# Optimization experiments

Measured on AMD Instinct MI355X. Metric: run time of the kernel, lower is better.

Reference implementation:

```python
import jax, jax.numpy as jnp
import numpy as np

N = 50000
E = 400000
F_IN = 128
HID = 64
HEADS = 4
OUT_HEADS = 4
N_CLS = 121
NEG_SLOPE = 0.2


def _gat_layer(x, src, dst, W, a_src, a_dst, b, heads, out_ch, concat):
    n = x.shape[0]
    xh = (x @ W).reshape(n, heads, out_ch)                      # [N,H,C]
    alpha_s = jnp.sum(xh * a_src, axis=-1)                      # [N,H]
    alpha_d = jnp.sum(xh * a_dst, axis=-1)                      # [N,H]
    logits = jax.nn.leaky_relu(alpha_s[src] + alpha_d[dst], NEG_SLOPE)  # [E,H]
    # numerically stable edge softmax per destination node
    m = jax.ops.segment_max(logits, dst, num_segments=n)        # [N,H]
    e = jnp.exp(logits - m[dst])                                # [E,H]
    denom = jax.ops.segment_sum(e, dst, num_segments=n)         # [N,H]
    alpha = e / (denom[dst] + 1e-16)                            # [E,H]
    msg = alpha[:, :, None] * xh[src]                           # [E,H,C]
    out = jax.ops.segment_sum(msg, dst, num_segments=n)         # [N,H,C]
    if concat:
        out = out.reshape(n, heads * out_ch)
    else:
        out = out.mean(axis=1)
    return out + b


def setup_inputs() -> dict:
    key = jax.random.key(0)
    ks = jax.random.split(key, 20)
    x = jax.random.normal(ks[0], (N, F_IN), dtype=jnp.float32)
    edge_index = jax.random.randint(ks[1], (2, E), 0, N, dtype=jnp.int32)
    s = lambda *sh: 1.0 / np.sqrt(sh[0])
    inp = {
        'x': x,
        'edge_index': edge_index,
        # conv1: F_IN -> HEADS*HID
        'W1': jax.random.normal(ks[2], (F_IN, HEADS * HID), jnp.float32) * s(F_IN),
        'a1_src': jax.random.normal(ks[3], (HEADS, HID), jnp.float32) * s(HID),
        'a1_dst': jax.random.normal(ks[4], (HEADS, HID), jnp.float32) * s(HID),
        'b1': jnp.zeros((HEADS * HID,), jnp.float32),
        'lin1_W': jax.random.normal(ks[5], (F_IN, HEADS * HID), jnp.float32) * s(F_IN),
        'lin1_b': jnp.zeros((HEADS * HID,), jnp.float32),
        # conv2: HEADS*HID -> HEADS*HID
        'W2': jax.random.normal(ks[6], (HEADS * HID, HEADS * HID), jnp.float32) * s(HEADS * HID),
        'a2_src': jax.random.normal(ks[7], (HEADS, HID), jnp.float32) * s(HID),
        'a2_dst': jax.random.normal(ks[8], (HEADS, HID), jnp.float32) * s(HID),
        'b2': jnp.zeros((HEADS * HID,), jnp.float32),
        # conv3: HEADS*HID -> N_CLS (mean over OUT_HEADS)
        'W3': jax.random.normal(ks[9], (HEADS * HID, OUT_HEADS * N_CLS), jnp.float32) * s(HEADS * HID),
        'a3_src': jax.random.normal(ks[10], (OUT_HEADS, N_CLS), jnp.float32) * s(N_CLS),
        'a3_dst': jax.random.normal(ks[11], (OUT_HEADS, N_CLS), jnp.float32) * s(N_CLS),
        'b3': jnp.zeros((N_CLS,), jnp.float32),
        'lin3_W': jax.random.normal(ks[12], (HEADS * HID, N_CLS), jnp.float32) * s(HEADS * HID),
        'lin3_b': jnp.zeros((N_CLS,), jnp.float32),
    }
    return inp


def reference(x, edge_index, W1, a1_src, a1_dst, b1, lin1_W, lin1_b,
              W2, a2_src, a2_dst, b2, W3, a3_src, a3_dst, b3, lin3_W, lin3_b):
    src, dst = edge_index[0], edge_index[1]
    h = _gat_layer(x, src, dst, W1, a1_src, a1_dst, b1, HEADS, HID, True) + (x @ lin1_W + lin1_b)
    h = jax.nn.elu(h)
    h = _gat_layer(h, src, dst, W2, a2_src, a2_dst, b2, HEADS, HID, True) + h  # residual skip (no lin2)
    h = jax.nn.elu(h)
    out = _gat_layer(h, src, dst, W3, a3_src, a3_dst, b3, OUT_HEADS, N_CLS, False) + (h @ lin3_W + lin3_b)
    return out
```

## Files before the change

kernel.cpp:

```cpp
#include <hip/hip_runtime.h>
#include <cstdint>
#include <cstddef>

#define F_IN 128
#define HC12 256
#define HC3 484
#define HC3P 488
#define NCLS 121

typedef unsigned short u16;
typedef unsigned int u32;
typedef __attribute__((ext_vector_type(8))) short short8;
typedef __attribute__((ext_vector_type(8))) __fp16 half8;
typedef __attribute__((ext_vector_type(4))) float float4v;

static __device__ __forceinline__ float lrelu(float x) { return x > 0.f ? x : 0.2f * x; }

static __device__ __forceinline__ u16 f2h(float f) {
    union { __fp16 h; u16 u; } v; v.h = (__fp16)f; return v.u;
}
static __device__ __forceinline__ float h2f(u16 u) {
    union { u16 u; __fp16 h; } v; v.u = u; return (float)v.h;
}

static __device__ __forceinline__ void gload16(const u16* g, u16* l) {
    __builtin_amdgcn_global_load_lds((const __attribute__((address_space(1))) void*)g,
                                     (__attribute__((address_space(3))) void*)l,
                                     16, 0, 0);
}

__global__ void hist_kernel(const int* __restrict__ dst, int* __restrict__ deg, int E) {
    int e = blockIdx.x * 256 + threadIdx.x;
    if (e < E) atomicAdd(&deg[dst[e]], 1);
}

__global__ __launch_bounds__(1024) void scan_kernel(const int* __restrict__ deg,
                                                    int* __restrict__ rowp, int N) {
    __shared__ int swave[16];
    __shared__ int s_carry;
    int tid = threadIdx.x;
    int w = tid >> 6, lane = tid & 63;
    if (tid == 0) { rowp[0] = 0; s_carry = 0; }
    __syncthreads();
    for (int base = 0; base < N; base += 4096) {
        int i0 = base + tid * 4;
        int v0 = (i0     < N) ? deg[i0]     : 0;
        int v1 = (i0 + 1 < N) ? deg[i0 + 1] : 0;
        int v2 = (i0 + 2 < N) ? deg[i0 + 2] : 0;
        int v3 = (i0 + 3 < N) ? deg[i0 + 3] : 0;
        int t = v0 + v1 + v2 + v3;
        int sc = t;
#pragma unroll
        for (int off = 1; off < 64; off <<= 1) {
            int u = __shfl_up(sc, off, 64);
            if (lane >= off) sc += u;
        }
        if (lane == 63) swave[w] = sc;
        __syncthreads();
        if (w == 0) {
            int ws = (lane < 16) ? swave[lane] : 0;
#pragma unroll
            for (int off = 1; off < 16; off <<= 1) {
                int u = __shfl_up(ws, off, 64);
                if (lane >= off) ws += u;
            }
            if (lane < 16) swave[lane] = ws;
        }
        __syncthreads();
        int carry = s_carry;
        int tb = carry + ((w > 0) ? swave[w - 1] : 0) + sc - t;
        if (i0     < N) rowp[i0 + 1] = tb + v0;
        if (i0 + 1 < N) rowp[i0 + 2] = tb + v0 + v1;
        if (i0 + 2 < N) rowp[i0 + 3] = tb + v0 + v1 + v2;
        if (i0 + 3 < N) rowp[i0 + 4] = tb + t;
        __syncthreads();
        if (tid == 1023) s_carry = carry + swave[15];
        __syncthreads();
    }
}

__global__ void scatter_kernel(const int* __restrict__ src, const int* __restrict__ dst,
                               const int* __restrict__ rowp, int* __restrict__ cur,
                               int* __restrict__ col, int E) {
    int e = blockIdx.x * 256 + threadIdx.x;
    if (e < E) {
        int d = dst[e];
        int pos = rowp[d] + atomicAdd(&cur[d], 1);
        col[pos] = src[e];
    }
}

__global__ void cvtT_all_kernel(const float* W1, const float* l1W, const float* W2,
                                const float* W3, const float* l3W,
                                u16* C1, u16* C2, u16* C3) {
    int i = blockIdx.x * 256 + threadIdx.x;
    const float* B; u16* o; int K, N;
    if (i < 32768)       { B = W1;  o = C1;             K = 128; N = 256; }
    else if (i < 65536)  { B = l1W; o = C1 + 256 * 128; K = 128; N = 256; i -= 32768; }
    else if (i < 131072) { B = W2;  o = C2;             K = 256; N = 256; i -= 65536; }
    else if (i < 254976) { B = W3;  o = C3;             K = 256; N = 484; i -= 131072; }
    else if (i < 285952) { B = l3W; o = C3 + 484 * 256; K = 256; N = 121; i -= 254976; }
    else return;
    int n = i % N, k = i / N;
    o[(size_t)n * K + k] = f2h(B[(size_t)k * N + n]);
}

__global__ __launch_bounds__(256) void xcvt_kernel(const float* __restrict__ x,
                                                   u16* __restrict__ o, int total8) {
    int i = blockIdx.x * 256 + threadIdx.x;
    if (i >= total8) return;
    const float4* p = (const float4*)(x + (size_t)i * 8);
    float4 a = p[0], b = p[1];
    union { u16 u[8]; short8 v; } r;
    r.u[0] = f2h(a.x); r.u[1] = f2h(a.y); r.u[2] = f2h(a.z); r.u[3] = f2h(a.w);
    r.u[4] = f2h(b.x); r.u[5] = f2h(b.y); r.u[6] = f2h(b.z); r.u[7] = f2h(b.w);
    *(short8*)(o + (size_t)i * 8) = r.v;
}

#define BM 128
#define BN 128
#define BK 32

__global__ __launch_bounds__(256, 3) void gemm_f16(const u16* __restrict__ A16,
                                                   const u16* __restrict__ BT,
                                                   int M, int K, int Ntot,
                                                   int nx, int ny,
                                                   int Nb, u16* __restrict__ Cb, int strideB,
                                                   int pad121,
                                                   float* __restrict__ Cf,
                                                   const float* __restrict__ biasf, int strideF) {
    __shared__ __align__(16) u16 sA[BM * BK];
    __shared__ __align__(16) u16 sB[BN * BK];
    int tid = threadIdx.x;
    int wave = tid >> 6, lane = tid & 63;
    int wr = wave >> 1, wc = wave & 1;

    int bid = blockIdx.x;
    int G = nx * 8;
    int g = bid / G;
    int rem = ny - g * 8;
    int rb, cb;
    if (rem >= 8) {
        int r = bid - g * G;
        rb = g * 8 + (r & 7);
        cb = r >> 3;
    } else {
        int t = bid - g * G;
        rb = g * 8 + t % rem;
        cb = t / rem;
    }
    int m0 = rb * BM, n0 = cb * BN;

    int fm = lane & 15;
    int q = lane >> 4;

    int srow = lane >> 2;
    int sch = (lane & 3) * 8;
    u16* lA0 = &sA[(wave * 32) * BK];
    u16* lA1 = &sA[(wave * 32 + 16) * BK];
    u16* lB0 = &sB[(wave * 32) * BK];
    u16* lB1 = &sB[(wave * 32 + 16) * BK];
    int ar0 = min(m0 + wave * 32 + srow, M - 1);
    int ar1 = min(m0 + wave * 32 + 16 + srow, M - 1);
    int br0 = min(n0 + wave * 32 + srow, Ntot - 1);
    int br1 = min(n0 + wave * 32 + 16 + srow, Ntot - 1);

    float4v acc[4][4];
#pragma unroll
    for (int i = 0; i < 4; i++)
#pragma unroll
        for (int j = 0; j < 4; j++) acc[i][j] = (float4v){0.f, 0.f, 0.f, 0.f};

    for (int kc = 0; kc < K; kc += BK) {
        gload16(&A16[(size_t)ar0 * K + kc + sch], lA0);
        gload16(&A16[(size_t)ar1 * K + kc + sch], lA1);
        gload16(&BT[(size_t)br0 * K + kc + sch], lB0);
        gload16(&BT[(size_t)br1 * K + kc + sch], lB1);
        __syncthreads();

        half8 ah[4];
#pragma unroll
        for (int mi = 0; mi < 4; mi++)
            ah[mi] = *(const half8*)&sA[(wr * 64 + mi * 16 + fm) * BK + q * 8];
#pragma unroll
        for (int ni = 0; ni < 4; ni++) {
            half8 bh = *(const half8*)&sB[(wc * 64 + ni * 16 + fm) * BK + q * 8];
#pragma unroll
            for (int mi = 0; mi < 4; mi++)
                acc[mi][ni] = __builtin_amdgcn_mfma_f32_16x16x32_f16(ah[mi], bh, acc[mi][ni], 0, 0, 0);
        }
        __syncthreads();
    }

#pragma unroll
    for (int mi = 0; mi < 4; mi++) {
#pragma unroll
        for (int ni = 0; ni < 4; ni++) {
            int colg = n0 + wc * 64 + ni * 16 + fm;
            if (colg >= Ntot) continue;
            int cg = colg;
            if (pad121 && colg < Nb) {
                int hh = (colg * 1084) >> 17;
                cg = colg + hh;
            }
#pragma unroll
            for (int r = 0; r < 4; r++) {
                int rowg = m0 + wr * 64 + mi * 16 + q * 4 + r;
                if (rowg >= M) continue;
                float v = acc[mi][ni][r];
                if (colg < Nb) {
                    Cb[(size_t)rowg * strideB + cg] = f2h(v);
                } else {
                    int cf = colg - Nb;
                    Cf[(size_t)rowg * strideF + cf] = v + biasf[cf];
                }
            }
        }
    }
}

__global__ __launch_bounds__(256) void alpha_wave_256(const u16* __restrict__ xh,
                                                      const float* __restrict__ a_s,
                                                      const float* __restrict__ a_d,
                                                      float* __restrict__ as_o,
                                                      float* __restrict__ ad_o, int N) {
    int lane = threadIdx.x & 63;
    int n = blockIdx.x * 4 + (threadIdx.x >> 6);
    if (n >= N) return;
    int c = lane * 4;
    uint2 v = *(const uint2*)&xh[(size_t)n * HC12 + c];
    float4 s4 = *(const float4*)&a_s[c];
    float4 d4 = *(const float4*)&a_d[c];
    float x0 = h2f((u16)(v.x & 0xffff)), x1 = h2f((u16)(v.x >> 16));
    float x2 = h2f((u16)(v.y & 0xffff)), x3 = h2f((u16)(v.y >> 16));
    float ss = x0 * s4.x + x1 * s4.y + x2 * s4.z + x3 * s4.w;
    float sd = x0 * d4.x + x1 * d4.y + x2 * d4.z + x3 * d4.w;
#pragma unroll
    for (int o = 1; o < 16; o <<= 1) {
        ss += __shfl_xor(ss, o, 64);
        sd += __shfl_xor(sd, o, 64);
    }
    if ((lane & 15) == 0) {
        as_o[n * 4 + (lane >> 4)] = ss;
        ad_o[n * 4 + (lane >> 4)] = sd;
    }
}

__global__ __launch_bounds__(256) void alpha3_wave(const u16* __restrict__ xh3,
                                                   const float* __restrict__ a_s,
                                                   const float* __restrict__ a_d,
                                                   float* __restrict__ as_o,
                                                   float* __restrict__ ad_o, int N) {
    int lane = threadIdx.x & 63;
    int n = blockIdx.x * 4 + (threadIdx.x >> 6);
    if (n >= N) return;
    int l = min(lane, 60);
    int c0 = 2 * l;
    float m0 = (lane < 61) ? 1.f : 0.f;
    float m1 = (lane < 61 && c0 + 1 < NCLS) ? 1.f : 0.f;
    int d1 = (c0 + 1 < NCLS) ? 1 : 0;
    const u16* row = xh3 + (size_t)n * HC3P;
    float ss[4], sd[4];
#pragma unroll
    for (int h = 0; h < 4; h++) {
        u32 v = *(const u32*)&row[h * 122 + c0];
        float x0 = h2f((u16)(v & 0xffff)) * m0;
        float x1 = h2f((u16)(v >> 16)) * m1;
        int i0 = h * NCLS + c0;
        ss[h] = x0 * a_s[i0] + x1 * a_s[i0 + d1];
        sd[h] = x0 * a_d[i0] + x1 * a_d[i0 + d1];
    }
#pragma unroll
    for (int o = 1; o < 64; o <<= 1) {
#pragma unroll
        for (int h = 0; h < 4; h++) {
            ss[h] += __shfl_xor(ss[h], o, 64);
            sd[h] += __shfl_xor(sd[h], o, 64);
        }
    }
    if (lane == 0) {
#pragma unroll
        for (int h = 0; h < 4; h++) {
            as_o[n * 4 + h] = ss[h];
            ad_o[n * 4 + h] = sd[h];
        }
    }
}

__global__ __launch_bounds__(256) void stats_alpha_kernel(const int* __restrict__ rowp,
                                                          const int* __restrict__ col,
                                                          const float* __restrict__ asrc,
                                                          const float* __restrict__ adst,
                                                          float* __restrict__ alphaE, int N) {
    int i = blockIdx.x * 256 + threadIdx.x;
    if (i >= N * 4) return;
    int n = i >> 2, h = i & 3;
    int r0 = rowp[n], r1 = rowp[n + 1];
    float ad = adst[i];
    float m = -3.4e38f, s = 0.f;
    for (int e = r0; e < r1; e++) {
        int sc = col[e];
        float l = lrelu(asrc[sc * 4 + h] + ad);
        float nm = fmaxf(m, l);
        s = s * __expf(m - nm) + __expf(l - nm);
        m = nm;
    }
    float rd = 1.f / (s + 1e-16f);
    for (int e = r0; e < r1; e++) {
        int sc = col[e];
        float l = lrelu(asrc[sc * 4 + h] + ad);
        alphaE[(size_t)e * 4 + h] = __expf(l - m) * rd;
    }
}

__global__ __launch_bounds__(256) void agg_wave_256(const u16* __restrict__ xh,
                                                    const int* __restrict__ rowp,
                                                    const int* __restrict__ col,
                                                    const float* __restrict__ alphaE,
                                                    const float* __restrict__ bias,
                                                    const float* __restrict__ res,
                                                    float* __restrict__ outf,
                                                    u16* __restrict__ out16, int N) {
    int lane = threadIdx.x & 63;
    int n = blockIdx.x * 4 + (threadIdx.x >> 6);
    if (n >= N) return;
    int r0 = rowp[n], r1 = rowp[n + 1];
    int c = lane * 4;
    int h = lane >> 4;
    float a0 = 0.f, a1 = 0.f, a2 = 0.f, a3 = 0.f;
    for (int kb = r0; kb < r1; kb += 16) {
        int cn = min(16, r1 - kb);
        int cidx = col[kb + (lane & 15)];
        float alv = alphaE[(size_t)kb * 4 + lane];
#pragma unroll 4
        for (int k = 0; k < cn; k++) {
            int src = __shfl(cidx, k, 64);
            float al = __shfl(alv, k * 4 + h, 64);
            uint2 v = *(const uint2*)&xh[(size_t)src * HC12 + c];
            a0 += al * h2f((u16)(v.x & 0xffff));
            a1 += al * h2f((u16)(v.x >> 16));
            a2 += al * h2f((u16)(v.y & 0xffff));
            a3 += al * h2f((u16)(v.y >> 16));
        }
    }
    float4 bv = *(const float4*)&bias[c];
    float4 rv = *(const float4*)&res[(size_t)n * HC12 + c];
    float v0 = a0 + bv.x + rv.x;
    float v1 = a1 + bv.y + rv.y;
    float v2 = a2 + bv.z + rv.z;
    float v3 = a3 + bv.w + rv.w;
    float e0 = v0 > 0.f ? v0 : expm1f(v0);
    float e1 = v1 > 0.f ? v1 : expm1f(v1);
    float e2 = v2 > 0.f ? v2 : expm1f(v2);
    float e3 = v3 > 0.f ? v3 : expm1f(v3);
    if (outf) {
        float4 o4; o4.x = e0; o4.y = e1; o4.z = e2; o4.w = e3;
        *(float4*)&outf[(size_t)n * HC12 + c] = o4;
    }
    union { u16 u[4]; uint2 v; } p;
    p.u[0] = f2h(e0); p.u[1] = f2h(e1); p.u[2] = f2h(e2); p.u[3] = f2h(e3);
    *(uint2*)&out16[(size_t)n * HC12 + c] = p.v;
}

__global__ __launch_bounds__(256) void agg_wave_out(const u16* __restrict__ xh3,
                                                    const int* __restrict__ rowp,
                                                    const int* __restrict__ col,
                                                    const float* __restrict__ alphaE,
                                                    const float* __restrict__ b3,
                                                    const float* __restrict__ lin3,
                                                    float* __restrict__ out, int N) {
    int lane = threadIdx.x & 63;
    int n = blockIdx.x * 4 + (threadIdx.x >> 6);
    if (n >= N) return;
    int r0 = rowp[n], r1 = rowp[n + 1];
    int l = min(lane, 60);
    int c0 = 2 * l;
    float acc[4][2];
#pragma unroll
    for (int h = 0; h < 4; h++) { acc[h][0] = 0.f; acc[h][1] = 0.f; }
    for (int kb = r0; kb < r1; kb += 16) {
        int cn = min(16, r1 - kb);
        int cidx = col[kb + (lane & 15)];
        float alv = alphaE[(size_t)kb * 4 + lane];
#pragma unroll 4
        for (int k = 0; k < cn; k++) {
            int src = __shfl(cidx, k, 64);
            float al0 = __shfl(alv, k * 4 + 0, 64);
            float al1 = __shfl(alv, k * 4 + 1, 64);
            float al2 = __shfl(alv, k * 4 + 2, 64);
            float al3 = __shfl(alv, k * 4 + 3, 64);
            const u16* row = xh3 + (size_t)src * HC3P + c0;
            u32 v0 = *(const u32*)&row[0];
            u32 v1 = *(const u32*)&row[122];
            u32 v2 = *(const u32*)&row[244];
            u32 v3 = *(const u32*)&row[366];
            acc[0][0] += al0 * h2f((u16)(v0 & 0xffff));
            acc[0][1] += al0 * h2f((u16)(v0 >> 16));
            acc[1][0] += al1 * h2f((u16)(v1 & 0xffff));
            acc[1][1] += al1 * h2f((u16)(v1 >> 16));
            acc[2][0] += al2 * h2f((u16)(v2 & 0xffff));
            acc[2][1] += al2 * h2f((u16)(v2 >> 16));
            acc[3][0] += al3 * h2f((u16)(v3 & 0xffff));
            acc[3][1] += al3 * h2f((u16)(v3 >> 16));
        }
    }
    if (lane < 61) {
        float o0 = 0.25f * (acc[0][0] + acc[1][0] + acc[2][0] + acc[3][0])
                   + b3[c0] + lin3[(size_t)n * NCLS + c0];
        out[(size_t)n * NCLS + c0] = o0;
        if (c0 + 1 < NCLS) {
            float o1 = 0.25f * (acc[0][1] + acc[1][1] + acc[2][1] + acc[3][1])
                       + b3[c0 + 1] + lin3[(size_t)n * NCLS + c0 + 1];
            out[(size_t)n * NCLS + c0 + 1] = o1;
        }
    }
}

extern "C" void kernel_launch(void* const* d_in, const int* in_sizes, int n_in,
                              void* d_out, int out_size, void* d_ws, size_t ws_size,
                              hipStream_t stream) {
    const float* x   = (const float*)d_in[0];
    const int*   ei  = (const int*)d_in[1];
    const float* W1  = (const float*)d_in[2];
    const float* a1s = (const float*)d_in[3];
    const float* a1d = (const float*)d_in[4];
    const float* b1  = (const float*)d_in[5];
    const float* l1W = (const float*)d_in[6];
    const float* l1b = (const float*)d_in[7];
    const float* W2  = (const float*)d_in[8];
    const float* a2s = (const float*)d_in[9];
    const float* a2d = (const float*)d_in[10];
    const float* b2  = (const float*)d_in[11];
    const float* W3  = (const float*)d_in[12];
    const float* a3s = (const float*)d_in[13];
    const float* a3d = (const float*)d_in[14];
    const float* b3  = (const float*)d_in[15];
    const float* l3W = (const float*)d_in[16];
    const float* l3b = (const float*)d_in[17];

    const int N = in_sizes[0] / F_IN;
    const int E = in_sizes[1] / 2;
    const int* srcv = ei;
    const int* dstv = ei + E;

    char* ws = (char*)d_ws;
    size_t off = 0;
    auto alloc = [&](size_t bytes) -> char* {
        char* p = ws + off;
        off += (bytes + 255) & ~(size_t)255;
        return p;
    };
    u16*   xh   = (u16*)alloc((size_t)N * HC3P * 2 + 256);
    u16*   x16  = (u16*)alloc((size_t)N * F_IN * 2);
    u16*   h1f  = (u16*)alloc((size_t)N * HC12 * 2);
    u16*   h2f  = (u16*)alloc((size_t)N * HC12 * 2);
    float* h1   = (float*)alloc((size_t)N * HC12 * 4);
    float* lin  = (float*)alloc((size_t)N * NCLS * 4);
    float* as_  = (float*)alloc((size_t)N * 4 * 4);
    float* ad_  = (float*)alloc((size_t)N * 4 * 4);
    int* rowp   = (int*)alloc((size_t)(N + 1) * 4);
    int* degc   = (int*)alloc((size_t)N * 4);
    int* cur    = (int*)alloc((size_t)N * 4);
    int* col    = (int*)alloc((size_t)E * 4 + 256);
    float* alphaE = (float*)alloc((size_t)E * 4 * 4 + 256);
    u16* C1 = (u16*)alloc((size_t)512 * 128 * 2);
    u16* C2 = (u16*)alloc((size_t)256 * 256 * 2);
    u16* C3 = (u16*)alloc((size_t)605 * 256 * 2);
    (void)ws_size; (void)n_in; (void)out_size;

    hipMemsetAsync(degc, 0, (size_t)N * 4, stream);
    hipMemsetAsync(cur, 0, (size_t)N * 4, stream);
    hist_kernel<<<(E + 255) / 256, 256, 0, stream>>>(dstv, degc, E);
    scan_kernel<<<1, 1024, 0, stream>>>(degc, rowp, N);
    scatter_kernel<<<(E + 255) / 256, 256, 0, stream>>>(srcv, dstv, rowp, cur, col, E);

    cvtT_all_kernel<<<(285952 + 255) / 256, 256, 0, stream>>>(W1, l1W, W2, W3, l3W, C1, C2, C3);
    xcvt_kernel<<<(N * F_IN / 8 + 255) / 256, 256, 0, stream>>>(x, x16, N * F_IN / 8);

    int ny = (N + BM - 1) / BM;
    int sgrid = (N * 4 + 255) / 256;
    int wgrid = (N + 3) / 4;

    gemm_f16<<<4 * ny, 256, 0, stream>>>(x16, C1, N, F_IN, 512, 4, ny,
                                         256, xh, 256, 0, h1, l1b, 256);
    alpha_wave_256<<<wgrid, 256, 0, stream>>>(xh, a1s, a1d, as_, ad_, N);
    stats_alpha_kernel<<<sgrid, 256, 0, stream>>>(rowp, col, as_, ad_, alphaE, N);
    agg_wave_256<<<wgrid, 256, 0, stream>>>(xh, rowp, col, alphaE, b1, h1, h1, h1f, N);

    gemm_f16<<<2 * ny, 256, 0, stream>>>(h1f, C2, N, HC12, 256, 2, ny,
                                         256, xh, 256, 0, nullptr, nullptr, 0);
    alpha_wave_256<<<wgrid, 256, 0, stream>>>(xh, a2s, a2d, as_, ad_, N);
    stats_alpha_kernel<<<sgrid, 256, 0, stream>>>(rowp, col, as_, ad_, alphaE, N);
    agg_wave_256<<<wgrid, 256, 0, stream>>>(xh, rowp, col, alphaE, b2, h1, nullptr, h2f, N);

    gemm_f16<<<5 * ny, 256, 0, stream>>>(h2f, C3, N, HC12, 605, 5, ny,
                                         484, xh, HC3P, 1, lin, l3b, NCLS);
    alpha3_wave<<<wgrid, 256, 0, stream>>>(xh, a3s, a3d, as_, ad_, N);
    stats_alpha_kernel<<<sgrid, 256, 0, stream>>>(rowp, col, as_, ad_, alphaE, N);
    agg_wave_out<<<wgrid, 256, 0, stream>>>(xh, rowp, col, alphaE, b3, lin, (float*)d_out, N);
}
```

Measured before the change: 539.2 us.

## Store skip/residual tensors in fp16 and widen aggregation gathers to 16-byte loads

The lin1 and lin3 skip outputs are now written by the GEMM as fp16 instead of fp32. The layer-2 residual reuses the fp16 h1f buffer rather than a separate fp32 h1 copy, which removes the extra fp32 write and read. The layer-3 xh layout is padded to 128 columns per head (stride 512), so alpha3 and the output aggregation can use aligned uint4 loads with one head per 16-lane group. The layers 1–2 aggregation splits each wave into two halves that process alternating edges with 8 channels per lane, then combines them with a shuffle. The trade-off is lower precision in the residual and skip paths, plus some wasted padded bandwidth in layer 3.

```diff
diff --git a/kernel.cpp b/kernel.cpp
--- a/kernel.cpp
+++ b/kernel.cpp
@@ -4,9 +4,9 @@
 
 #define F_IN 128
 #define HC12 256
-#define HC3 484
-#define HC3P 488
+#define HC3P 512
 #define NCLS 121
+#define L3STR 128
 
 typedef unsigned short u16;
 typedef unsigned int u32;
@@ -127,7 +127,7 @@
                                                    int nx, int ny,
                                                    int Nb, u16* __restrict__ Cb, int strideB,
                                                    int pad121,
-                                                   float* __restrict__ Cf,
+                                                   u16* __restrict__ Cf16,
                                                    const float* __restrict__ biasf, int strideF) {
     __shared__ __align__(16) u16 sA[BM * BK];
     __shared__ __align__(16) u16 sB[BN * BK];
@@ -201,7 +201,7 @@
             int cg = colg;
             if (pad121 && colg < Nb) {
                 int hh = (colg * 1084) >> 17;
-                cg = colg + hh;
+                cg = colg + 7 * hh;
             }
 #pragma unroll
             for (int r = 0; r < 4; r++) {
@@ -212,7 +212,7 @@
                     Cb[(size_t)rowg * strideB + cg] = f2h(v);
                 } else {
                     int cf = colg - Nb;
-                    Cf[(size_t)rowg * strideF + cf] = v + biasf[cf];
+                    Cf16[(size_t)rowg * strideF + cf] = f2h(v + biasf[cf]);
                 }
             }
         }
@@ -251,39 +251,32 @@
                                                    const float* __restrict__ a_d,
                                                    float* __restrict__ as_o,
                                                    float* __restrict__ ad_o, int N) {
-    int lane = threadIdx.x & 63;
+    int l = threadIdx.x & 63;
     int n = blockIdx.x * 4 + (threadIdx.x >> 6);
     if (n >= N) return;
-    int l = min(lane, 60);
-    int c0 = 2 * l;
-    float m0 = (lane < 61) ? 1.f : 0.f;
-    float m1 = (lane < 61 && c0 + 1 < NCLS) ? 1.f : 0.f;
-    int d1 = (c0 + 1 < NCLS) ? 1 : 0;
-    const u16* row = xh3 + (size_t)n * HC3P;
-    float ss[4], sd[4];
-#pragma unroll
-    for (int h = 0; h < 4; h++) {
-        u32 v = *(const u32*)&row[h * 122 + c0];
-        float x0 = h2f((u16)(v & 0xffff)) * m0;
-        float x1 = h2f((u16)(v >> 16)) * m1;
-        int i0 = h * NCLS + c0;
-        ss[h] = x0 * a_s[i0] + x1 * a_s[i0 + d1];
-        sd[h] = x0 * a_d[i0] + x1 * a_d[i0 + d1];
-    }
-#pragma unroll
-    for (int o = 1; o < 64; o <<= 1) {
-#pragma unroll
-        for (int h = 0; h < 4; h++) {
-            ss[h] += __shfl_xor(ss[h], o, 64);
-            sd[h] += __shfl_xor(sd[h], o, 64);
-        }
-    }
-    if (lane == 0) {
-#pragma unroll
-        for (int h = 0; h < 4; h++) {
-            as_o[n * 4 + h] = ss[h];
-            ad_o[n * 4 + h] = sd[h];
-        }
+    int h = l >> 4, li = l & 15;
+    int c0 = li * 8;
+    uint4 v = *(const uint4*)&xh3[(size_t)n * HC3P + l * 8];
+    u32 ww[4] = {v.x, v.y, v.z, v.w};
+    float ss = 0.f, sd = 0.f;
+#pragma unroll
+    for (int j = 0; j < 8; j++) {
+        int cc = c0 + j;
+        if (cc < NCLS) {
+            u16 raw = (u16)((ww[j >> 1] >> ((j & 1) * 16)) & 0xffff);
+            float xf = h2f(raw);
+            ss += xf * a_s[h * NCLS + cc];
+            sd += xf * a_d[h * NCLS + cc];
+        }
+    }
+#pragma unroll
+    for (int o = 1; o < 16; o <<= 1) {
+        ss += __shfl_xor(ss, o, 64);
+        sd += __shfl_xor(sd, o, 64);
+    }
+    if (li == 0) {
+        as_o[n * 4 + h] = ss;
+        ad_o[n * 4 + h] = sd;
     }
 }
 
@@ -318,48 +311,57 @@
                                                     const int* __restrict__ col,
                                                     const float* __restrict__ alphaE,
                                                     const float* __restrict__ bias,
-                                                    const float* __restrict__ res,
-                                                    float* __restrict__ outf,
+                                                    const u16* __restrict__ res16,
                                                     u16* __restrict__ out16, int N) {
-    int lane = threadIdx.x & 63;
+    int l = threadIdx.x & 63;
     int n = blockIdx.x * 4 + (threadIdx.x >> 6);
     if (n >= N) return;
     int r0 = rowp[n], r1 = rowp[n + 1];
-    int c = lane * 4;
-    int h = lane >> 4;
-    float a0 = 0.f, a1 = 0.f, a2 = 0.f, a3 = 0.f;
+    int s = l >> 5, li = l & 31;
+    int c = li * 8;
+    int h = li >> 3;
+    float acc[8] = {0.f, 0.f, 0.f, 0.f, 0.f, 0.f, 0.f, 0.f};
     for (int kb = r0; kb < r1; kb += 16) {
         int cn = min(16, r1 - kb);
-        int cidx = col[kb + (lane & 15)];
-        float alv = alphaE[(size_t)kb * 4 + lane];
+        int cidx = col[kb + (l & 15)];
+        float alv = alphaE[(size_t)kb * 4 + l];
+        int npair = (cn + 1) >> 1;
 #pragma unroll 4
-        for (int k = 0; k < cn; k++) {
-            int src = __shfl(cidx, k, 64);
-            float al = __shfl(alv, k * 4 + h, 64);
-            uint2 v = *(const uint2*)&xh[(size_t)src * HC12 + c];
-            a0 += al * h2f((u16)(v.x & 0xffff));
-            a1 += al * h2f((u16)(v.x >> 16));
-            a2 += al * h2f((u16)(v.y & 0xffff));
-            a3 += al * h2f((u16)(v.y >> 16));
-        }
-    }
-    float4 bv = *(const float4*)&bias[c];
-    float4 rv = *(const float4*)&res[(size_t)n * HC12 + c];
-    float v0 = a0 + bv.x + rv.x;
-    float v1 = a1 + bv.y + rv.y;
-    float v2 = a2 + bv.z + rv.z;
-    float v3 = a3 + bv.w + rv.w;
-    float e0 = v0 > 0.f ? v0 : expm1f(v0);
-    float e1 = v1 > 0.f ? v1 : expm1f(v1);
-    float e2 = v2 > 0.f ? v2 : expm1f(v2);
-    float e3 = v3 > 0.f ? v3 : expm1f(v3);
-    if (outf) {
-        float4 o4; o4.x = e0; o4.y = e1; o4.z = e2; o4.w = e3;
-        *(float4*)&outf[(size_t)n * HC12 + c] = o4;
-    }
-    union { u16 u[4]; uint2 v; } p;
-    p.u[0] = f2h(e0); p.u[1] = f2h(e1); p.u[2] = f2h(e2); p.u[3] = f2h(e3);
-    *(uint2*)&out16[(size_t)n * HC12 + c] = p.v;
+        for (int k = 0; k < npair; k++) {
+            int e = 2 * k + s;
+            int em = e < cn ? e : cn - 1;
+            int src = __shfl(cidx, em, 64);
+            float al = __shfl(alv, em * 4 + h, 64);
+            if (e >= cn) al = 0.f;
+            uint4 v = *(const uint4*)&xh[(size_t)src * HC12 + c];
+            acc[0] += al * h2f((u16)(v.x & 0xffff));
+            acc[1] += al * h2f((u16)(v.x >> 16));
+            acc[2] += al * h2f((u16)(v.y & 0xffff));
+            acc[3] += al * h2f((u16)(v.y >> 16));
+            acc[4] += al * h2f((u16)(v.z & 0xffff));
+            acc[5] += al * h2f((u16)(v.z >> 16));
+            acc[6] += al * h2f((u16)(v.w & 0xffff));
+            acc[7] += al * h2f((u16)(v.w >> 16));
+        }
+    }
+#pragma unroll
+    for (int j = 0; j < 8; j++) acc[j] += __shfl_xor(acc[j], 32, 64);
+    if (l < 32) {
+        uint4 rv = *(const uint4*)&res16[(size_t)n * HC12 + c];
+        u32 rw[4] = {rv.x, rv.y, rv.z, rv.w};
+        float4 b0 = *(const float4*)&bias[c];
+        float4 b1v = *(const float4*)&bias[c + 4];
+        float bb[8] = {b0.x, b0.y, b0.z, b0.w, b1v.x, b1v.y, b1v.z, b1v.w};
+        union { u16 u[8]; uint4 v; } p;
+#pragma unroll
+        for (int j = 0; j < 8; j++) {
+            float rf = h2f((u16)((rw[j >> 1] >> ((j & 1) * 16)) & 0xffff));
+            float vv = acc[j] + bb[j] + rf;
+            float ev = vv > 0.f ? vv : expm1f(vv);
+            p.u[j] = f2h(ev);
+        }
+        *(uint4*)&out16[(size_t)n * HC12 + c] = p.v;
+    }
 }
 
 __global__ __launch_bounds__(256) void agg_wave_out(const u16* __restrict__ xh3,
@@ -367,51 +369,49 @@
                                                     const int* __restrict__ col,
                                                     const float* __restrict__ alphaE,
                                                     const float* __restrict__ b3,
-                                                    const float* __restrict__ lin3,
+                                                    const u16* __restrict__ lin3h,
                                                     float* __restrict__ out, int N) {
-    int lane = threadIdx.x & 63;
+    int l = threadIdx.x & 63;
     int n = blockIdx.x * 4 + (threadIdx.x >> 6);
     if (n >= N) return;
     int r0 = rowp[n], r1 = rowp[n + 1];
-    int l = min(lane, 60);
-    int c0 = 2 * l;
-    float acc[4][2];
-#pragma unroll
-    for (int h = 0; h < 4; h++) { acc[h][0] = 0.f; acc[h][1] = 0.f; }
+    int h = l >> 4;
+    float acc[8] = {0.f, 0.f, 0.f, 0.f, 0.f, 0.f, 0.f, 0.f};
     for (int kb = r0; kb < r1; kb += 16) {
         int cn = min(16, r1 - kb);
-        int cidx = col[kb + (lane & 15)];
-        float alv = alphaE[(size_t)kb * 4 + lane];
+        int cidx = col[kb + (l & 15)];
+        float alv = alphaE[(size_t)kb * 4 + l];
 #pragma unroll 4
         for (int k = 0; k < cn; k++) {
             int src = __shfl(cidx, k, 64);
-            float al0 = __shfl(alv, k * 4 + 0, 64);
-            float al1 = __shfl(alv, k * 4 + 1, 64);
-            float al2 = __shfl(alv, k * 4 + 2, 64);
-            float al3 = __shfl(alv, k * 4 + 3, 64);
-            const u16* row = xh3 + (size_t)src * HC3P + c0;
-            u32 v0 = *(const u32*)&row[0];
-            u32 v1 = *(const u32*)&row[122];
-            u32 v2 = *(const u32*)&row[244];
-            u32 v3 = *(const u32*)&row[366];
-            acc[0][0] += al0 * h2f((u16)(v0 & 0xffff));
-            acc[0][1] += al0 * h2f((u16)(v0 >> 16));
-            acc[1][0] += al1 * h2f((u16)(v1 & 0xffff));
-            acc[1][1] += al1 * h2f((u16)(v1 >> 16));
-            acc[2][0] += al2 * h2f((u16)(v2 & 0xffff));
-            acc[2][1] += al2 * h2f((u16)(v2 >> 16));
-            acc[3][0] += al3 * h2f((u16)(v3 & 0xffff));
-            acc[3][1] += al3 * h2f((u16)(v3 >> 16));
-        }
-    }
-    if (lane < 61) {
-        float o0 = 0.25f * (acc[0][0] + acc[1][0] + acc[2][0] + acc[3][0])
-                   + b3[c0] + lin3[(size_t)n * NCLS + c0];
-        out[(size_t)n * NCLS + c0] = o0;
-        if (c0 + 1 < NCLS) {
-            float o1 = 0.25f * (acc[0][1] + acc[1][1] + acc[2][1] + acc[3][1])
-                       + b3[c0 + 1] + lin3[(size_t)n * NCLS + c0 + 1];
-            out[(size_t)n * NCLS + c0 + 1] = o1;
+            float al = __shfl(alv, k * 4 + h, 64);
+            uint4 v = *(const uint4*)&xh3[(size_t)src * HC3P + l * 8];
+            acc[0] += al * h2f((u16)(v.x & 0xffff));
+            acc[1] += al * h2f((u16)(v.x >> 16));
+            acc[2] += al * h2f((u16)(v.y & 0xffff));
+            acc[3] += al * h2f((u16)(v.y >> 16));
+            acc[4] += al * h2f((u16)(v.z & 0xffff));
+            acc[5] += al * h2f((u16)(v.z >> 16));
+            acc[6] += al * h2f((u16)(v.w & 0xffff));
+            acc[7] += al * h2f((u16)(v.w >> 16));
+        }
+    }
+#pragma unroll
+    for (int j = 0; j < 8; j++) {
+        acc[j] += __shfl_xor(acc[j], 16, 64);
+        acc[j] += __shfl_xor(acc[j], 32, 64);
+    }
+    if (l < 16) {
+        uint4 lv = *(const uint4*)&lin3h[(size_t)n * L3STR + l * 8];
+        u32 lw[4] = {lv.x, lv.y, lv.z, lv.w};
+        int c0 = l * 8;
+#pragma unroll
+        for (int j = 0; j < 8; j++) {
+            int cc = c0 + j;
+            if (cc < NCLS) {
+                float lf = h2f((u16)((lw[j >> 1] >> ((j & 1) * 16)) & 0xffff));
+                out[(size_t)n * NCLS + cc] = 0.25f * acc[j] + b3[cc] + lf;
+            }
         }
     }
 }
@@ -450,18 +450,18 @@
         off += (bytes + 255) & ~(size_t)255;
         return p;
     };
-    u16*   xh   = (u16*)alloc((size_t)N * HC3P * 2 + 256);
-    u16*   x16  = (u16*)alloc((size_t)N * F_IN * 2);
-    u16*   h1f  = (u16*)alloc((size_t)N * HC12 * 2);
-    u16*   h2f  = (u16*)alloc((size_t)N * HC12 * 2);
-    float* h1   = (float*)alloc((size_t)N * HC12 * 4);
-    float* lin  = (float*)alloc((size_t)N * NCLS * 4);
-    float* as_  = (float*)alloc((size_t)N * 4 * 4);
-    float* ad_  = (float*)alloc((size_t)N * 4 * 4);
-    int* rowp   = (int*)alloc((size_t)(N + 1) * 4);
-    int* degc   = (int*)alloc((size_t)N * 4);
-    int* cur    = (int*)alloc((size_t)N * 4);
-    int* col    = (int*)alloc((size_t)E * 4 + 256);
+    u16*   xh    = (u16*)alloc((size_t)N * HC3P * 2 + 256);
+    u16*   x16   = (u16*)alloc((size_t)N * F_IN * 2);
+    u16*   h1f   = (u16*)alloc((size_t)N * HC12 * 2);
+    u16*   h2f   = (u16*)alloc((size_t)N * HC12 * 2);
+    u16*   lin1h = (u16*)alloc((size_t)N * HC12 * 2);
+    u16*   lin3h = (u16*)alloc((size_t)N * L3STR * 2);
+    float* as_   = (float*)alloc((size_t)N * 4 * 4);
+    float* ad_   = (float*)alloc((size_t)N * 4 * 4);
+    int* rowp    = (int*)alloc((size_t)(N + 1) * 4);
+    int* degc    = (int*)alloc((size_t)N * 4);
+    int* cur     = (int*)alloc((size_t)N * 4);
+    int* col     = (int*)alloc((size_t)E * 4 + 256);
     float* alphaE = (float*)alloc((size_t)E * 4 * 4 + 256);
     u16* C1 = (u16*)alloc((size_t)512 * 128 * 2);
     u16* C2 = (u16*)alloc((size_t)256 * 256 * 2);
@@ -482,20 +482,20 @@
     int wgrid = (N + 3) / 4;
 
     gemm_f16<<<4 * ny, 256, 0, stream>>>(x16, C1, N, F_IN, 512, 4, ny,
-                                         256, xh, 256, 0, h1, l1b, 256);
+                                         256, xh, 256, 0, lin1h, l1b, 256);
     alpha_wave_256<<<wgrid, 256, 0, stream>>>(xh, a1s, a1d, as_, ad_, N);
     stats_alpha_kernel<<<sgrid, 256, 0, stream>>>(rowp, col, as_, ad_, alphaE, N);
-    agg_wave_256<<<wgrid, 256, 0, stream>>>(xh, rowp, col, alphaE, b1, h1, h1, h1f, N);
+    agg_wave_256<<<wgrid, 256, 0, stream>>>(xh, rowp, col, alphaE, b1, lin1h, h1f, N);
 
     gemm_f16<<<2 * ny, 256, 0, stream>>>(h1f, C2, N, HC12, 256, 2, ny,
                                          256, xh, 256, 0, nullptr, nullptr, 0);
     alpha_wave_256<<<wgrid, 256, 0, stream>>>(xh, a2s, a2d, as_, ad_, N);
     stats_alpha_kernel<<<sgrid, 256, 0, stream>>>(rowp, col, as_, ad_, alphaE, N);
-    agg_wave_256<<<wgrid, 256, 0, stream>>>(xh, rowp, col, alphaE, b2, h1, nullptr, h2f, N);
+    agg_wave_256<<<wgrid, 256, 0, stream>>>(xh, rowp, col, alphaE, b2, h1f, h2f, N);
 
     gemm_f16<<<5 * ny, 256, 0, stream>>>(h2f, C3, N, HC12, 605, 5, ny,
-                                         484, xh, HC3P, 1, lin, l3b, NCLS);
+                                         484, xh, HC3P, 1, lin3h, l3b, L3STR);
     alpha3_wave<<<wgrid, 256, 0, stream>>>(xh, a3s, a3d, as_, ad_, N);
     stats_alpha_kernel<<<sgrid, 256, 0, stream>>>(rowp, col, as_, ad_, alphaE, N);
-    agg_wave_out<<<wgrid, 256, 0, stream>>>(xh, rowp, col, alphaE, b3, lin, (float*)d_out, N);
-}
+    agg_wave_out<<<wgrid, 256, 0, stream>>>(xh, rowp, col, alphaE, b3, lin3h, (float*)d_out, N);
+}
```

New measurement: 586.8 us. +8.8%, slower.
